# Kernel optimization log

Measured on AMD Instinct MI355X. Metric: run time of the kernel, lower is better.

## Reference

```python
import jax, jax.numpy as jnp
import numpy as np
import math

B, N, DQ, DK, DV, H = 8, 1024, 512, 512, 512, 8


def setup_inputs() -> dict:
    key = jax.random.key(0)
    ks = jax.random.split(key, 9)
    s = 0.02
    return {
        "Q": jax.random.normal(ks[0], (B, N, DQ), jnp.float32),
        "K": jax.random.normal(ks[1], (B, N, DK), jnp.float32),
        "mask": jax.random.bernoulli(ks[2], 0.9, (B, N)).astype(jnp.float32),
        "Wq": jax.random.normal(ks[3], (DQ, DV), jnp.float32) * s,
        "bq": jnp.zeros((DV,), jnp.float32),
        "Wk": jax.random.normal(ks[4], (DK, DV), jnp.float32) * s,
        "bk": jnp.zeros((DV,), jnp.float32),
        "Wv": jax.random.normal(ks[5], (DK, DV), jnp.float32) * s,
        "bv": jnp.zeros((DV,), jnp.float32),
        "Wo": jax.random.normal(ks[6], (DV, DV), jnp.float32) * s,
        "bo": jnp.zeros((DV,), jnp.float32),
    }


def reference(Q, K, mask, Wq, bq, Wk, bk, Wv, bv, Wo, bo):
    b, n, _ = Q.shape
    dV = Wq.shape[1]
    dh = dV // H
    scale = 1.0 / math.sqrt(dV)
    m = mask[..., None]                      # [B,N,1]
    Qp = (Q @ Wq + bq) * m                   # [B,N,dV]
    Kp = (K @ Wk + bk) * m
    Vp = (K @ Wv + bv) * m
    # torch.cat(x.split(dh,2),0) == head-major stacking -> keep as [H,B,N,dh]
    q = Qp.reshape(b, n, H, dh).transpose(2, 0, 1, 3)
    k = Kp.reshape(b, n, H, dh).transpose(2, 0, 1, 3)
    v = Vp.reshape(b, n, H, dh).transpose(2, 0, 1, 3)
    S = jnp.einsum('hbnd,hbmd->hbnm', q, k) * scale   # [H,B,N,N]
    mx = jnp.max(S, axis=3, keepdims=True)            # unmasked row max (faithful)
    m1 = mask[None, :, :, None]                       # [1,B,N,1]
    m2 = mask[None, :, None, :]                       # [1,B,1,N]
    num = jnp.exp((S - mx) * m1 * m2) * m1 * m2
    A = num / (jnp.sum(num, axis=3, keepdims=True) + 1e-16)
    O = q + jnp.einsum('hbnm,hbmd->hbnd', A, v)       # residual on Q_
    O = O.transpose(1, 2, 0, 3).reshape(b, n, dV)     # un-split heads
    O = O + jax.nn.relu((O @ Wo + bo) * m)
    return O
```

## Files before the change

kernel.cpp:

```cpp
#include <hip/hip_runtime.h>

typedef short bf16x8 __attribute__((ext_vector_type(8)));
typedef float f32x4 __attribute__((ext_vector_type(4)));
typedef float f32x16 __attribute__((ext_vector_type(16)));

#define MFMA16(a, b, c) __builtin_amdgcn_mfma_f32_16x16x32_bf16((a), (b), (c), 0, 0, 0)
#define MFMA32(a, b, c) __builtin_amdgcn_mfma_f32_32x32x16_bf16((a), (b), (c), 0, 0, 0)

#define GLOAD_LDS16(g, l)                                              \
  __builtin_amdgcn_global_load_lds(                                    \
      (const __attribute__((address_space(1))) unsigned int*)(g),      \
      (__attribute__((address_space(3))) unsigned int*)(l), 16, 0, 0)

__device__ __forceinline__ unsigned short f2b(float f) {
  union { float f; unsigned int u; } x; x.f = f;
  unsigned int r = x.u + 0x7FFFu + ((x.u >> 16) & 1u);
  return (unsigned short)(r >> 16);
}
__device__ __forceinline__ float b2f(unsigned short h) {
  union { unsigned int u; float f; } x; x.u = ((unsigned int)h) << 16;
  return x.f;
}
__device__ __forceinline__ unsigned int cvtpk(float lo, float hi) {
  unsigned int r;
  asm("v_cvt_pk_bf16_f32 %0, %1, %2" : "=v"(r) : "v"(lo), "v"(hi));
  return r;
}
__device__ __forceinline__ short cvt1(float x) {
  return (short)(unsigned short)cvtpk(x, x);
}
__device__ __forceinline__ float vexp2(float x) {
  float r;
  asm("v_exp_f32 %0, %1" : "=v"(r) : "v"(x));
  return r;
}

#define SCALE2 0.06375870724f

__global__ __launch_bounds__(256) void wtrans_kernel(
    const float* __restrict__ Wq, const float* __restrict__ Wk,
    const float* __restrict__ Wv, const float* __restrict__ Wo,
    short* __restrict__ Wt) {
  __shared__ float tile[64][65];
  const int z = blockIdx.z;
  const float* W = (z == 0) ? Wq : (z == 1) ? Wk : (z == 2) ? Wv : Wo;
  const float ws = (z == 1) ? SCALE2 : 1.0f;
  const int k0 = blockIdx.x * 64, n0 = blockIdx.y * 64;
  const int t = threadIdx.x;
  const int r = t >> 4, cc = (t & 15) * 4;
#pragma unroll
  for (int it = 0; it < 4; ++it) {
    int row = r + it * 16;
    const float4 v = *(const float4*)(W + (k0 + row) * 512 + n0 + cc);
    tile[row][cc + 0] = v.x; tile[row][cc + 1] = v.y;
    tile[row][cc + 2] = v.z; tile[row][cc + 3] = v.w;
  }
  __syncthreads();
  short* out = Wt + z * (512 * 512);
#pragma unroll
  for (int it = 0; it < 4; ++it) {
    int nrow = r + it * 16;
    unsigned int u0 = cvtpk(tile[cc + 0][nrow] * ws, tile[cc + 1][nrow] * ws);
    unsigned int u1 = cvtpk(tile[cc + 2][nrow] * ws, tile[cc + 3][nrow] * ws);
    uint2 uv; uv.x = u0; uv.y = u1;
    *(uint2*)(out + (n0 + nrow) * 512 + k0 + cc) = uv;
  }
}

__global__ __launch_bounds__(256) void cvt_kernel(
    const float* __restrict__ Q, const float* __restrict__ K,
    const float* __restrict__ mask,
    short* __restrict__ Qb, short* __restrict__ Kb, short* __restrict__ mbf) {
  if (blockIdx.y == 0 && blockIdx.x < 4) {
    int i = (blockIdx.x * 256 + threadIdx.x) * 8;
    float4 a = *(const float4*)(mask + i);
    float4 bb = *(const float4*)(mask + i + 4);
    unsigned int m0 = (a.x != 0.f) ? 0x3F80u : 0u;
    unsigned int m1 = (a.y != 0.f) ? 0x3F80u : 0u;
    unsigned int m2 = (a.z != 0.f) ? 0x3F80u : 0u;
    unsigned int m3 = (a.w != 0.f) ? 0x3F80u : 0u;
    unsigned int m4 = (bb.x != 0.f) ? 0x3F80u : 0u;
    unsigned int m5 = (bb.y != 0.f) ? 0x3F80u : 0u;
    unsigned int m6 = (bb.z != 0.f) ? 0x3F80u : 0u;
    unsigned int m7 = (bb.w != 0.f) ? 0x3F80u : 0u;
    uint4 mm;
    mm.x = m0 | (m1 << 16); mm.y = m2 | (m3 << 16);
    mm.z = m4 | (m5 << 16); mm.w = m6 | (m7 << 16);
    *(uint4*)(mbf + i) = mm;
  }
  const float* src = blockIdx.y ? K : Q;
  short* dst = blockIdx.y ? Kb : Qb;
  int i = (blockIdx.x * 256 + threadIdx.x) * 8;
  float4 v0 = *(const float4*)(src + i);
  float4 v1 = *(const float4*)(src + i + 4);
  uint2 a, b;
  a.x = cvtpk(v0.x, v0.y); a.y = cvtpk(v0.z, v0.w);
  b.x = cvtpk(v1.x, v1.y); b.y = cvtpk(v1.z, v1.w);
  *(uint2*)(dst + i) = a;
  *(uint2*)(dst + i + 4) = b;
}

__device__ __forceinline__ void gemm_bf16_core(
    const short* __restrict__ A, const short* __restrict__ Wt,
    short* Lb, int m0, int t, f32x4 acc[4][4]) {
  const int lane = t & 63, w = t >> 6;
  const int c = lane & 15, g = lane >> 4;
  const int wr = w >> 1, wc = w & 1;
  const int lr = lane >> 3;
  const int sswz = ((lane & 7) ^ lr) << 3;
  const int swc = (c & 7) << 3;
  short* Al = Lb;
  short* Bl = Lb + 8192;

  for (int kt = 0; kt < 8; ++kt) {
#pragma unroll
    for (int it = 0; it < 4; ++it) {
      int row = w * 32 + it * 8;
      GLOAD_LDS16(A + (size_t)(m0 + row + lr) * 512 + kt * 64 + sswz, Al + row * 64);
      GLOAD_LDS16(Wt + (size_t)(row + lr) * 512 + kt * 64 + sswz, Bl + row * 64);
    }
    __syncthreads();
    __builtin_amdgcn_s_setprio(1);
#pragma unroll
    for (int kc = 0; kc < 2; ++kc) {
      bf16x8 af[4], bfr[4];
#pragma unroll
      for (int mi = 0; mi < 4; ++mi) {
        int r = wr * 64 + mi * 16 + c;
        af[mi] = *(const bf16x8*)(Al + r * 64 + ((kc * 32 + 8 * g) ^ swc));
      }
#pragma unroll
      for (int ni = 0; ni < 4; ++ni) {
        int r = wc * 64 + ni * 16 + c;
        bfr[ni] = *(const bf16x8*)(Bl + r * 64 + ((kc * 32 + 8 * g) ^ swc));
      }
#pragma unroll
      for (int mi = 0; mi < 4; ++mi)
#pragma unroll
        for (int ni = 0; ni < 4; ++ni)
          acc[mi][ni] = MFMA16(af[mi], bfr[ni], acc[mi][ni]);
    }
    __builtin_amdgcn_s_setprio(0);
    __syncthreads();
  }
}

__global__ __launch_bounds__(256) void proj2_kernel(
    const short* __restrict__ Qb, const short* __restrict__ Kb,
    const short* __restrict__ Wt4,
    const float* __restrict__ bq, const float* __restrict__ bk, const float* __restrict__ bv,
    const float* __restrict__ maskf,
    short* __restrict__ Qp, short* __restrict__ Kp, short* __restrict__ Vt) {
  __shared__ short Lbuf[16384];
  const int by = blockIdx.y;
  const int m0 = blockIdx.x * 128;
  const int t = threadIdx.x;
  const short* A;
  const short* Wt;
  const float* bias;
  int nbase;
  if (by < 4) { A = Qb; nbase = by * 128; Wt = Wt4 + nbase * 512; bias = bq; }
  else if (by < 8) { A = Kb; nbase = (by - 4) * 128; Wt = Wt4 + 262144 + nbase * 512; bias = bk; }
  else { A = Kb; nbase = (by - 8) * 128; Wt = Wt4 + 524288 + nbase * 512; bias = bv; }
  const float bscale = (by >= 4 && by < 8) ? SCALE2 : 1.0f;

  const f32x4 zz = {0.f, 0.f, 0.f, 0.f};
  f32x4 acc[4][4];
#pragma unroll
  for (int mi = 0; mi < 4; ++mi)
#pragma unroll
    for (int ni = 0; ni < 4; ++ni) acc[mi][ni] = zz;
  gemm_bf16_core(A, Wt, Lbuf, m0, t, acc);

  const int lane = t & 63, w = t >> 6;
  const int c = lane & 15, g = lane >> 4;
  const int wr = w >> 1, wc = w & 1;
  float mk[4][4];
#pragma unroll
  for (int mi = 0; mi < 4; ++mi) {
    int mbase = m0 + wr * 64 + mi * 16 + 4 * g;
#pragma unroll
    for (int i = 0; i < 4; ++i) mk[mi][i] = maskf[mbase + i];
  }
  float bval[4];
#pragma unroll
  for (int ni = 0; ni < 4; ++ni) bval[ni] = bias[nbase + wc * 64 + ni * 16 + c] * bscale;

  if (by < 8) {
#pragma unroll
    for (int ni = 0; ni < 4; ++ni) {
      int nloc = wc * 64 + ni * 16 + c;
#pragma unroll
      for (int mi = 0; mi < 4; ++mi) {
#pragma unroll
        for (int i = 0; i < 4; ++i) {
          int mloc = wr * 64 + mi * 16 + 4 * g + i;
          float v = (acc[mi][ni][i] + bval[ni]) * mk[mi][i];
          Lbuf[mloc * 128 + (nloc ^ ((mloc & 7) << 3))] = cvt1(v);
        }
      }
    }
    __syncthreads();
    short* outp = (by < 4) ? Qp : Kp;
    const int rrow = t >> 4, rcol = (t & 15) * 8;
#pragma unroll
    for (int p = 0; p < 8; ++p) {
      int m = p * 16 + rrow;
      bf16x8 vv = *(const bf16x8*)(Lbuf + m * 128 + (rcol ^ ((m & 7) << 3)));
      *(bf16x8*)(outp + (size_t)(m0 + m) * 512 + nbase + rcol) = vv;
    }
  } else {
#pragma unroll
    for (int ni = 0; ni < 4; ++ni) {
      int nloc = wc * 64 + ni * 16 + c;
#pragma unroll
      for (int mi = 0; mi < 4; ++mi) {
        int mloc4 = wr * 64 + mi * 16 + 4 * g;
        unsigned int lo = cvtpk((acc[mi][ni][0] + bval[ni]) * mk[mi][0],
                                (acc[mi][ni][1] + bval[ni]) * mk[mi][1]);
        unsigned int hi = cvtpk((acc[mi][ni][2] + bval[ni]) * mk[mi][2],
                                (acc[mi][ni][3] + bval[ni]) * mk[mi][3]);
        int ma = (mloc4 & 15) + (((mloc4 >> 4) ^ (nloc & 7)) << 4);
        uint2 uv; uv.x = lo; uv.y = hi;
        *(uint2*)(Lbuf + nloc * 128 + ma) = uv;
      }
    }
    __syncthreads();
    const int rrow = t >> 4, rcol = (t & 15) * 8;
#pragma unroll
    for (int p = 0; p < 8; ++p) {
      int n = p * 16 + rrow;
      int ma = (rcol & 8) + (((rcol >> 4) ^ (n & 7)) << 4);
      bf16x8 vv = *(const bf16x8*)(Lbuf + n * 128 + ma);
      int d = nbase + n;
      int hh = d >> 6, dd = d & 63;
      int mg = m0 + rcol;
      int bi = mg >> 10, seq0 = mg & 1023;
      *(bf16x8*)(Vt + ((size_t)((bi * 8 + hh) * 64 + dd)) * 1024 + seq0) = vv;
    }
  }
}

__global__ __launch_bounds__(128) void attn5_kernel(
    const short* __restrict__ Qp, const short* __restrict__ Kp,
    const short* __restrict__ Vt, const float* __restrict__ mask,
    const short* __restrict__ mbf, short* __restrict__ Obb) {
  __shared__ short Kl[64 * 128];
  __shared__ short Vl[64 * 128];
  __shared__ short Ml[1024];
  const int t = threadIdx.x, lane = t & 63, w = t >> 6;
  const int q32 = lane & 31, hi = lane >> 5;
  const int hw = blockIdx.x;
  const int L = (hw & 7) * 128 + (hw >> 3);
  const int qt = L & 15, head = L >> 4;
  const int b = head & 7, h = head >> 3;
  const int n0 = qt * 64 + w * 32;

  const short* Kg = Kp + (size_t)(b * 1024) * 512 + h * 64;
  const short* Vg = Vt + (size_t)((b * 8 + h) * 64) * 1024;

  bf16x8 qf[4];
  {
    const short* qptr = Qp + ((size_t)(b * 1024 + n0 + q32) * 512 + h * 64 + 8 * hi);
#pragma unroll
    for (int kk = 0; kk < 4; ++kk) qf[kk] = *(const bf16x8*)(qptr + 16 * kk);
  }

  auto STAGE = [&](int kvt) {
    const int kr = kvt * 128;
#pragma unroll
    for (int it = 0; it < 8; ++it) {
      int rb = it * 8 + w * 4;
      int r2 = rb + (lane >> 4);
      int sx = (lane & 15) ^ (r2 & 15);
      int kv = 2 * r2 + (sx >> 3);
      int j = sx & 7;
      GLOAD_LDS16(Kg + (size_t)(kr + kv) * 512 + j * 8, Kl + rb * 128);
    }
#pragma unroll
    for (int it = 0; it < 8; ++it) {
      int rb = it * 8 + w * 4;
      int d = rb + (lane >> 4);
      int sx = (lane & 15) ^ (d & 15);
      GLOAD_LDS16(Vg + (size_t)d * 1024 + kr + sx * 8, Vl + rb * 128);
    }
  };

  GLOAD_LDS16(mbf + b * 1024 + w * 512 + lane * 8, Ml + w * 512);
  STAGE(0);

  f32x16 o0, o1, suma;
#pragma unroll
  for (int e = 0; e < 16; ++e) { o0[e] = 0.f; o1[e] = 0.f; suma[e] = 0.f; }

#pragma unroll 1
  for (int kvt = 0; kvt < 8; ++kvt) {
    asm volatile("s_waitcnt vmcnt(0)" ::: "memory");
    __builtin_amdgcn_sched_barrier(0);
    __builtin_amdgcn_s_barrier();
    __builtin_amdgcn_sched_barrier(0);

    bf16x8 ka[2][2][4], va[2][2][4], mo[2][4];
#pragma unroll
    for (int sub = 0; sub < 2; ++sub) {
#pragma unroll
      for (int nb = 0; nb < 2; ++nb)
#pragma unroll
        for (int kk = 0; kk < 4; ++kk) {
          int kvr = sub * 64 + 32 * nb + q32;
          int r2 = kvr >> 1;
          int sx = (((kvr & 1) << 3) | (2 * kk + hi)) ^ (r2 & 15);
          ka[sub][nb][kk] = *(const bf16x8*)(Kl + r2 * 128 + sx * 8);
        }
#pragma unroll
      for (int ds = 0; ds < 2; ++ds)
#pragma unroll
        for (int kk = 0; kk < 4; ++kk) {
          int d = 32 * ds + q32;
          int sx = (sub * 8 + 2 * kk + hi) ^ (d & 15);
          va[sub][ds][kk] = *(const bf16x8*)(Vl + d * 128 + sx * 8);
        }
#pragma unroll
      for (int kk = 0; kk < 4; ++kk)
        mo[sub][kk] = *(const bf16x8*)(Ml + kvt * 128 + sub * 64 + 16 * kk + 8 * hi);
    }

    __builtin_amdgcn_sched_barrier(0);
    asm volatile("s_waitcnt lgkmcnt(0)" ::: "memory");
    __builtin_amdgcn_sched_barrier(0);
    __builtin_amdgcn_s_barrier();
    __builtin_amdgcn_sched_barrier(0);
    if (kvt < 7) STAGE(kvt + 1);
    __builtin_amdgcn_sched_barrier(0);

#pragma unroll
    for (int sub = 0; sub < 2; ++sub) {
      f32x16 s0, s1;
#pragma unroll
      for (int e = 0; e < 16; ++e) { s0[e] = 0.f; s1[e] = 0.f; }
      __builtin_amdgcn_s_setprio(1);
#pragma unroll
      for (int kk = 0; kk < 4; ++kk) s0 = MFMA32(ka[sub][0][kk], qf[kk], s0);
#pragma unroll
      for (int kk = 0; kk < 4; ++kk) s1 = MFMA32(ka[sub][1][kk], qf[kk], s1);
      __builtin_amdgcn_s_setprio(0);

      f32x16 p0, p1;
#pragma unroll
      for (int e = 0; e < 16; ++e) p0[e] = vexp2(s0[e]);
#pragma unroll
      for (int e = 0; e < 16; ++e) p1[e] = vexp2(s1[e]);

      bf16x8 pf[4];
#pragma unroll
      for (int kk = 0; kk < 4; ++kk) {
        const int m_ = kk & 1;
        unsigned int w01a, w01b, w23a, w23b;
        if (kk < 2) {
          w01a = cvtpk(p0[8 * m_ + 0], p0[8 * m_ + 1]);
          w01b = cvtpk(p0[8 * m_ + 2], p0[8 * m_ + 3]);
          w23a = cvtpk(p0[8 * m_ + 4], p0[8 * m_ + 5]);
          w23b = cvtpk(p0[8 * m_ + 6], p0[8 * m_ + 7]);
        } else {
          w01a = cvtpk(p1[8 * m_ + 0], p1[8 * m_ + 1]);
          w01b = cvtpk(p1[8 * m_ + 2], p1[8 * m_ + 3]);
          w23a = cvtpk(p1[8 * m_ + 4], p1[8 * m_ + 5]);
          w23b = cvtpk(p1[8 * m_ + 6], p1[8 * m_ + 7]);
        }
        unsigned int x0 = hi ? w01a : w23a;
        unsigned int x1 = hi ? w01b : w23b;
        unsigned int g0 = (unsigned int)__shfl_xor((int)x0, 32);
        unsigned int g1 = (unsigned int)__shfl_xor((int)x1, 32);
        union { unsigned int u[4]; bf16x8 v; } pu;
        pu.u[0] = hi ? g0 : w01a;
        pu.u[1] = hi ? g1 : w01b;
        pu.u[2] = hi ? w23a : g0;
        pu.u[3] = hi ? w23b : g1;
        pf[kk] = pu.v;
      }

      __builtin_amdgcn_s_setprio(1);
#pragma unroll
      for (int kk = 0; kk < 4; ++kk) o0 = MFMA32(va[sub][0][kk], pf[kk], o0);
#pragma unroll
      for (int kk = 0; kk < 4; ++kk) o1 = MFMA32(va[sub][1][kk], pf[kk], o1);
#pragma unroll
      for (int kk = 0; kk < 4; ++kk) suma = MFMA32(mo[sub][kk], pf[kk], suma);
      __builtin_amdgcn_s_setprio(0);
    }
  }

  short* Tw = Kl + w * 2304;
  const float inv = __builtin_amdgcn_rcpf(suma[0] + 1e-16f);
#pragma unroll
  for (int rr = 0; rr < 4; ++rr) {
    unsigned int lo0 = cvtpk(o0[4 * rr + 0] * inv, o0[4 * rr + 1] * inv);
    unsigned int hi0 = cvtpk(o0[4 * rr + 2] * inv, o0[4 * rr + 3] * inv);
    uint2 uv0; uv0.x = lo0; uv0.y = hi0;
    *(uint2*)(Tw + q32 * 68 + 8 * rr + 4 * hi) = uv0;
    unsigned int lo1 = cvtpk(o1[4 * rr + 0] * inv, o1[4 * rr + 1] * inv);
    unsigned int hi1 = cvtpk(o1[4 * rr + 2] * inv, o1[4 * rr + 3] * inv);
    uint2 uv1; uv1.x = lo1; uv1.y = hi1;
    *(uint2*)(Tw + q32 * 68 + 32 + 8 * rr + 4 * hi) = uv1;
  }
  asm volatile("s_waitcnt lgkmcnt(0)" ::: "memory");
  __builtin_amdgcn_sched_barrier(0);

  const int erow = lane >> 1, ecs = (lane & 1) * 8;
  const float mk1 = mask[b * 1024 + n0 + erow];
#pragma unroll
  for (int it = 0; it < 4; ++it) {
    int col = ecs + it * 16;
    bf16x8 av = *(const bf16x8*)(Tw + erow * 68 + col);
    const short* qptr = Qp + (size_t)(b * 1024 + n0 + erow) * 512 + h * 64 + col;
    bf16x8 qv = *(const bf16x8*)qptr;
    uint4 rr;
    rr.x = cvtpk(b2f((unsigned short)qv[0]) + mk1 * b2f((unsigned short)av[0]),
                 b2f((unsigned short)qv[1]) + mk1 * b2f((unsigned short)av[1]));
    rr.y = cvtpk(b2f((unsigned short)qv[2]) + mk1 * b2f((unsigned short)av[2]),
                 b2f((unsigned short)qv[3]) + mk1 * b2f((unsigned short)av[3]));
    rr.z = cvtpk(b2f((unsigned short)qv[4]) + mk1 * b2f((unsigned short)av[4]),
                 b2f((unsigned short)qv[5]) + mk1 * b2f((unsigned short)av[5]));
    rr.w = cvtpk(b2f((unsigned short)qv[6]) + mk1 * b2f((unsigned short)av[6]),
                 b2f((unsigned short)qv[7]) + mk1 * b2f((unsigned short)av[7]));
    *(uint4*)(Obb + (size_t)(b * 1024 + n0 + erow) * 512 + h * 64 + col) = rr;
  }
}

__global__ __launch_bounds__(256) void final2_kernel(
    const short* __restrict__ Obb,
    const short* __restrict__ Wto, const float* __restrict__ bo,
    const float* __restrict__ maskf, float* __restrict__ out) {
  __shared__ short Lbuf[16384];
  const int m0 = blockIdx.x * 128, n0 = blockIdx.y * 128;
  const int t = threadIdx.x;
  const f32x4 zz = {0.f, 0.f, 0.f, 0.f};
  f32x4 acc[4][4];
#pragma unroll
  for (int mi = 0; mi < 4; ++mi)
#pragma unroll
    for (int ni = 0; ni < 4; ++ni) acc[mi][ni] = zz;
  gemm_bf16_core(Obb, Wto + n0 * 512, Lbuf, m0, t, acc);

  const int lane = t & 63, w = t >> 6;
  const int c = lane & 15, g = lane >> 4;
  const int wr = w >> 1, wc = w & 1;
  float mk[4][4];
#pragma unroll
  for (int mi = 0; mi < 4; ++mi) {
    int mbase = m0 + wr * 64 + mi * 16 + 4 * g;
#pragma unroll
    for (int i = 0; i < 4; ++i) mk[mi][i] = maskf[mbase + i];
  }
#pragma unroll
  for (int ni = 0; ni < 4; ++ni) {
    int n = n0 + wc * 64 + ni * 16 + c;
    float bval = bo[n];
#pragma unroll
    for (int mi = 0; mi < 4; ++mi) {
      int mbase = m0 + wr * 64 + mi * 16 + 4 * g;
#pragma unroll
      for (int i = 0; i < 4; ++i) {
        float v = (acc[mi][ni][i] + bval) * mk[mi][i];
        v = fmaxf(v, 0.f);
        size_t off = (size_t)(mbase + i) * 512 + n;
        out[off] = b2f((unsigned short)Obb[off]) + v;
      }
    }
  }
}

extern "C" void kernel_launch(void* const* d_in, const int* in_sizes, int n_in,
                              void* d_out, int out_size, void* d_ws, size_t ws_size,
                              hipStream_t stream) {
  (void)in_sizes; (void)n_in; (void)out_size; (void)ws_size;
  const float* Q    = (const float*)d_in[0];
  const float* K    = (const float*)d_in[1];
  const float* mask = (const float*)d_in[2];
  const float* Wq   = (const float*)d_in[3];
  const float* bq   = (const float*)d_in[4];
  const float* Wk   = (const float*)d_in[5];
  const float* bk   = (const float*)d_in[6];
  const float* Wv   = (const float*)d_in[7];
  const float* bv   = (const float*)d_in[8];
  const float* Wo   = (const float*)d_in[9];
  const float* bo   = (const float*)d_in[10];

  char* ws = (char*)d_ws;
  const size_t MB = 1048576;
  short* Wt4 = (short*)ws;
  short* Qb  = (short*)(ws + 2 * MB);
  short* Kb  = (short*)(ws + 10 * MB);
  short* Qp  = (short*)(ws + 18 * MB);
  short* Kp  = (short*)(ws + 26 * MB);
  short* Vt  = (short*)(ws + 34 * MB);
  short* Obb = (short*)(ws + 42 * MB);
  short* mbf = (short*)(ws + 50 * MB);
  float* out = (float*)d_out;

  wtrans_kernel<<<dim3(8, 8, 4), 256, 0, stream>>>(Wq, Wk, Wv, Wo, Wt4);
  cvt_kernel<<<dim3(2048, 2), 256, 0, stream>>>(Q, K, mask, Qb, Kb, mbf);
  proj2_kernel<<<dim3(64, 12), 256, 0, stream>>>(Qb, Kb, Wt4, bq, bk, bv, mask, Qp, Kp, Vt);
  attn5_kernel<<<dim3(1024), 128, 0, stream>>>(Qp, Kp, Vt, mask, mbf, Obb);
  final2_kernel<<<dim3(64, 4), 256, 0, stream>>>(Obb, Wt4 + 3 * 262144, bo, mask, out);
}
```

Before: 92.60 us.

## Halve attention KV tile to 64 and split into two halves to cut registers

The attention kernel now stages 64 keys per iteration instead of 128, so there are twice as many loop iterations and the LDS buffers for K and V are half the size. Each iteration is processed in two 32-key halves that load their own K/V fragments, which shrinks the live register set. A launch-bounds minimum of 3 blocks per CU is added. The goal is higher occupancy and lower register and LDS pressure, paid for with more barriers, more staging rounds, and smaller MFMA batches between syncs.

```diff
diff --git a/kernel.cpp b/kernel.cpp
--- a/kernel.cpp
+++ b/kernel.cpp
@@ -241,12 +241,12 @@
   }
 }
 
-__global__ __launch_bounds__(128) void attn5_kernel(
+__global__ __launch_bounds__(128, 3) void attn6_kernel(
     const short* __restrict__ Qp, const short* __restrict__ Kp,
     const short* __restrict__ Vt, const float* __restrict__ mask,
     const short* __restrict__ mbf, short* __restrict__ Obb) {
-  __shared__ short Kl[64 * 128];
-  __shared__ short Vl[64 * 128];
+  __shared__ short Kl[32 * 128];
+  __shared__ short Vl[32 * 128];
   __shared__ short Ml[1024];
   const int t = threadIdx.x, lane = t & 63, w = t >> 6;
   const int q32 = lane & 31, hi = lane >> 5;
@@ -267,22 +267,20 @@
   }
 
   auto STAGE = [&](int kvt) {
-    const int kr = kvt * 128;
-#pragma unroll
-    for (int it = 0; it < 8; ++it) {
+    const int kr = kvt * 64;
+#pragma unroll
+    for (int it = 0; it < 4; ++it) {
       int rb = it * 8 + w * 4;
       int r2 = rb + (lane >> 4);
       int sx = (lane & 15) ^ (r2 & 15);
-      int kv = 2 * r2 + (sx >> 3);
-      int j = sx & 7;
-      GLOAD_LDS16(Kg + (size_t)(kr + kv) * 512 + j * 8, Kl + rb * 128);
-    }
-#pragma unroll
-    for (int it = 0; it < 8; ++it) {
+      GLOAD_LDS16(Kg + (size_t)(kr + 2 * r2 + (sx >> 3)) * 512 + (sx & 7) * 8, Kl + rb * 128);
+    }
+#pragma unroll
+    for (int it = 0; it < 4; ++it) {
       int rb = it * 8 + w * 4;
-      int d = rb + (lane >> 4);
-      int sx = (lane & 15) ^ (d & 15);
-      GLOAD_LDS16(Vg + (size_t)d * 1024 + kr + sx * 8, Vl + rb * 128);
+      int rv = rb + (lane >> 4);
+      int sx = (lane & 15) ^ (rv & 15);
+      GLOAD_LDS16(Vg + (size_t)(2 * rv + (sx >> 3)) * 1024 + kr + (sx & 7) * 8, Vl + rb * 128);
     }
   };
 
@@ -294,79 +292,67 @@
   for (int e = 0; e < 16; ++e) { o0[e] = 0.f; o1[e] = 0.f; suma[e] = 0.f; }
 
 #pragma unroll 1
-  for (int kvt = 0; kvt < 8; ++kvt) {
+  for (int kvt = 0; kvt < 16; ++kvt) {
     asm volatile("s_waitcnt vmcnt(0)" ::: "memory");
     __builtin_amdgcn_sched_barrier(0);
     __builtin_amdgcn_s_barrier();
     __builtin_amdgcn_sched_barrier(0);
 
-    bf16x8 ka[2][2][4], va[2][2][4], mo[2][4];
-#pragma unroll
-    for (int sub = 0; sub < 2; ++sub) {
-#pragma unroll
-      for (int nb = 0; nb < 2; ++nb)
+#pragma unroll
+    for (int half = 0; half < 2; ++half) {
+      bf16x8 ka[4], va[2][2], mo[2];
+      {
+        const int kvr = 32 * half + q32;
+        const int r2 = kvr >> 1;
 #pragma unroll
         for (int kk = 0; kk < 4; ++kk) {
-          int kvr = sub * 64 + 32 * nb + q32;
-          int r2 = kvr >> 1;
-          int sx = (((kvr & 1) << 3) | (2 * kk + hi)) ^ (r2 & 15);
-          ka[sub][nb][kk] = *(const bf16x8*)(Kl + r2 * 128 + sx * 8);
+          int sx = ((((kvr & 1) << 3) | (2 * kk + hi)) ^ (r2 & 15));
+          ka[kk] = *(const bf16x8*)(Kl + r2 * 128 + sx * 8);
         }
-#pragma unroll
-      for (int ds = 0; ds < 2; ++ds)
-#pragma unroll
-        for (int kk = 0; kk < 4; ++kk) {
-          int d = 32 * ds + q32;
-          int sx = (sub * 8 + 2 * kk + hi) ^ (d & 15);
-          va[sub][ds][kk] = *(const bf16x8*)(Vl + d * 128 + sx * 8);
+      }
+#pragma unroll
+      for (int ds = 0; ds < 2; ++ds) {
+        const int d = 32 * ds + q32;
+        const int rv = d >> 1;
+#pragma unroll
+        for (int ch = 0; ch < 2; ++ch) {
+          int sx = ((((d & 1) << 3) | (4 * half + 2 * ch + hi)) ^ (rv & 15));
+          va[ds][ch] = *(const bf16x8*)(Vl + rv * 128 + sx * 8);
         }
-#pragma unroll
-      for (int kk = 0; kk < 4; ++kk)
-        mo[sub][kk] = *(const bf16x8*)(Ml + kvt * 128 + sub * 64 + 16 * kk + 8 * hi);
-    }
-
-    __builtin_amdgcn_sched_barrier(0);
-    asm volatile("s_waitcnt lgkmcnt(0)" ::: "memory");
-    __builtin_amdgcn_sched_barrier(0);
-    __builtin_amdgcn_s_barrier();
-    __builtin_amdgcn_sched_barrier(0);
-    if (kvt < 7) STAGE(kvt + 1);
-    __builtin_amdgcn_sched_barrier(0);
-
-#pragma unroll
-    for (int sub = 0; sub < 2; ++sub) {
-      f32x16 s0, s1;
-#pragma unroll
-      for (int e = 0; e < 16; ++e) { s0[e] = 0.f; s1[e] = 0.f; }
+      }
+#pragma unroll
+      for (int ch = 0; ch < 2; ++ch)
+        mo[ch] = *(const bf16x8*)(Ml + kvt * 64 + 32 * half + 16 * ch + 8 * hi);
+
+      __builtin_amdgcn_sched_barrier(0);
+      asm volatile("s_waitcnt lgkmcnt(0)" ::: "memory");
+      __builtin_amdgcn_sched_barrier(0);
+      if (half == 1) {
+        __builtin_amdgcn_s_barrier();
+        __builtin_amdgcn_sched_barrier(0);
+        if (kvt < 15) STAGE(kvt + 1);
+        __builtin_amdgcn_sched_barrier(0);
+      }
+
+      f32x16 s0;
+#pragma unroll
+      for (int e = 0; e < 16; ++e) s0[e] = 0.f;
       __builtin_amdgcn_s_setprio(1);
 #pragma unroll
-      for (int kk = 0; kk < 4; ++kk) s0 = MFMA32(ka[sub][0][kk], qf[kk], s0);
-#pragma unroll
-      for (int kk = 0; kk < 4; ++kk) s1 = MFMA32(ka[sub][1][kk], qf[kk], s1);
+      for (int kk = 0; kk < 4; ++kk) s0 = MFMA32(ka[kk], qf[kk], s0);
       __builtin_amdgcn_s_setprio(0);
 
-      f32x16 p0, p1;
+      f32x16 p0;
 #pragma unroll
       for (int e = 0; e < 16; ++e) p0[e] = vexp2(s0[e]);
-#pragma unroll
-      for (int e = 0; e < 16; ++e) p1[e] = vexp2(s1[e]);
-
-      bf16x8 pf[4];
-#pragma unroll
-      for (int kk = 0; kk < 4; ++kk) {
-        const int m_ = kk & 1;
-        unsigned int w01a, w01b, w23a, w23b;
-        if (kk < 2) {
-          w01a = cvtpk(p0[8 * m_ + 0], p0[8 * m_ + 1]);
-          w01b = cvtpk(p0[8 * m_ + 2], p0[8 * m_ + 3]);
-          w23a = cvtpk(p0[8 * m_ + 4], p0[8 * m_ + 5]);
-          w23b = cvtpk(p0[8 * m_ + 6], p0[8 * m_ + 7]);
-        } else {
-          w01a = cvtpk(p1[8 * m_ + 0], p1[8 * m_ + 1]);
-          w01b = cvtpk(p1[8 * m_ + 2], p1[8 * m_ + 3]);
-          w23a = cvtpk(p1[8 * m_ + 4], p1[8 * m_ + 5]);
-          w23b = cvtpk(p1[8 * m_ + 6], p1[8 * m_ + 7]);
-        }
+
+      bf16x8 pf[2];
+#pragma unroll
+      for (int ch = 0; ch < 2; ++ch) {
+        unsigned int w01a = cvtpk(p0[8 * ch + 0], p0[8 * ch + 1]);
+        unsigned int w01b = cvtpk(p0[8 * ch + 2], p0[8 * ch + 3]);
+        unsigned int w23a = cvtpk(p0[8 * ch + 4], p0[8 * ch + 5]);
+        unsigned int w23b = cvtpk(p0[8 * ch + 6], p0[8 * ch + 7]);
         unsigned int x0 = hi ? w01a : w23a;
         unsigned int x1 = hi ? w01b : w23b;
         unsigned int g0 = (unsigned int)__shfl_xor((int)x0, 32);
@@ -376,16 +362,16 @@
         pu.u[1] = hi ? g1 : w01b;
         pu.u[2] = hi ? w23a : g0;
         pu.u[3] = hi ? w23b : g1;
-        pf[kk] = pu.v;
+        pf[ch] = pu.v;
       }
 
       __builtin_amdgcn_s_setprio(1);
 #pragma unroll
-      for (int kk = 0; kk < 4; ++kk) o0 = MFMA32(va[sub][0][kk], pf[kk], o0);
-#pragma unroll
-      for (int kk = 0; kk < 4; ++kk) o1 = MFMA32(va[sub][1][kk], pf[kk], o1);
-#pragma unroll
-      for (int kk = 0; kk < 4; ++kk) suma = MFMA32(mo[sub][kk], pf[kk], suma);
+      for (int ch = 0; ch < 2; ++ch) {
+        o0 = MFMA32(va[0][ch], pf[ch], o0);
+        o1 = MFMA32(va[1][ch], pf[ch], o1);
+        suma = MFMA32(mo[ch], pf[ch], suma);
+      }
       __builtin_amdgcn_s_setprio(0);
     }
   }
@@ -394,13 +380,12 @@
   const float inv = __builtin_amdgcn_rcpf(suma[0] + 1e-16f);
 #pragma unroll
   for (int rr = 0; rr < 4; ++rr) {
-    unsigned int lo0 = cvtpk(o0[4 * rr + 0] * inv, o0[4 * rr + 1] * inv);
-    unsigned int hi0 = cvtpk(o0[4 * rr + 2] * inv, o0[4 * rr + 3] * inv);
-    uint2 uv0; uv0.x = lo0; uv0.y = hi0;
+    uint2 uv0, uv1;
+    uv0.x = cvtpk(o0[4 * rr + 0] * inv, o0[4 * rr + 1] * inv);
+    uv0.y = cvtpk(o0[4 * rr + 2] * inv, o0[4 * rr + 3] * inv);
     *(uint2*)(Tw + q32 * 68 + 8 * rr + 4 * hi) = uv0;
-    unsigned int lo1 = cvtpk(o1[4 * rr + 0] * inv, o1[4 * rr + 1] * inv);
-    unsigned int hi1 = cvtpk(o1[4 * rr + 2] * inv, o1[4 * rr + 3] * inv);
-    uint2 uv1; uv1.x = lo1; uv1.y = hi1;
+    uv1.x = cvtpk(o1[4 * rr + 0] * inv, o1[4 * rr + 1] * inv);
+    uv1.y = cvtpk(o1[4 * rr + 2] * inv, o1[4 * rr + 3] * inv);
     *(uint2*)(Tw + q32 * 68 + 32 + 8 * rr + 4 * hi) = uv1;
   }
   asm volatile("s_waitcnt lgkmcnt(0)" ::: "memory");
@@ -501,6 +486,6 @@
   wtrans_kernel<<<dim3(8, 8, 4), 256, 0, stream>>>(Wq, Wk, Wv, Wo, Wt4);
   cvt_kernel<<<dim3(2048, 2), 256, 0, stream>>>(Q, K, mask, Qb, Kb, mbf);
   proj2_kernel<<<dim3(64, 12), 256, 0, stream>>>(Qb, Kb, Wt4, bq, bk, bv, mask, Qp, Kp, Vt);
-  attn5_kernel<<<dim3(1024), 128, 0, stream>>>(Qp, Kp, Vt, mask, mbf, Obb);
+  attn6_kernel<<<dim3(1024), 128, 0, stream>>>(Qp, Kp, Vt, mask, mbf, Obb);
   final2_kernel<<<dim3(64, 4), 256, 0, stream>>>(Obb, Wt4 + 3 * 262144, bo, mask, out);
 }
```

New measurement: 82.79 us. -10.6%, faster.
